# Kernel optimization log

Measured on AMD Instinct MI355X. Metric: run time of the kernel, lower is better.

## Reference

```python
import jax, jax.numpy as jnp
import numpy as np
from jax import lax

B, T = 64, 2048
ENC, DEC, ATT = 512, 1024, 128
NFILT, KSIZE = 32, 31
PAD = KSIZE // 2


def setup_inputs() -> dict:
    key = jax.random.key(0)
    ks = jax.random.split(key, 9)
    query = jax.random.normal(ks[0], (B, 1, DEC), dtype=jnp.float32)
    keys = jax.random.normal(ks[1], (B, T, ENC), dtype=jnp.float32)
    prev_weights = jax.random.uniform(ks[2], (B, T), dtype=jnp.float32)
    mask = jax.random.randint(ks[3], (B, T), 0, 2, dtype=jnp.int32)
    # params stored as [in, out] (transpose of torch Linear weight); same math
    W1 = jax.random.normal(ks[4], (ENC, ATT), dtype=jnp.float32) * (ENC ** -0.5)
    W2 = jax.random.normal(ks[5], (DEC, ATT), dtype=jnp.float32) * (DEC ** -0.5)
    V = jax.random.normal(ks[6], (ATT,), dtype=jnp.float32) * (ATT ** -0.5)
    conv_w = jax.random.normal(ks[7], (NFILT, 1, KSIZE), dtype=jnp.float32) * (KSIZE ** -0.5)
    loc_dense = jax.random.normal(ks[8], (NFILT, ATT), dtype=jnp.float32) * (NFILT ** -0.5)
    return {"query": query, "keys": keys, "prev_weights": prev_weights, "mask": mask,
            "W1": W1, "W2": W2, "V": V, "conv_w": conv_w, "loc_dense": loc_dense}


def reference(query, keys, prev_weights, mask, W1, W2, V, conv_w, loc_dense):
    proj_key = jnp.einsum('bte,ea->bta', keys, W1)          # [B,T,A]
    proj_query = jnp.einsum('bqd,da->bqa', query, W2)       # [B,1,A]
    # location conv: input [B,1,T], kernel [F,1,K], 'same' padding -> [B,F,T]
    loc_feat = lax.conv_general_dilated(prev_weights[:, None, :], conv_w,
                                        window_strides=(1,), padding=[(PAD, PAD)],
                                        dimension_numbers=('NCH', 'OIH', 'NCH'))
    proj_loc = jnp.einsum('bft,fa->bta', loc_feat, loc_dense)  # [B,T,A]
    scores = jnp.einsum('bta,a->bt', jnp.tanh(proj_key + proj_query + proj_loc), V)
    scores = jnp.where(mask == 0, -1e9, scores)
    weights = jax.nn.softmax(scores, axis=-1)                # [B,T]
    context = jnp.einsum('bt,bte->be', weights, keys)[:, None, :]  # [B,1,ENC]
    return context, weights
```

## Files before the change

### kernel.cpp

```cpp
#include <hip/hip_runtime.h>

typedef __attribute__((ext_vector_type(4))) float f32x4;
typedef __attribute__((ext_vector_type(8))) short bf16x8;

#define T_LEN 2048
#define ENC   512
#define DEC   1024
#define ATT   128
#define NB    64
#define BM    128
#define BK    32
#define NXB   (T_LEN / BM)
#define NSTEP 17

typedef unsigned int u32;
typedef __attribute__((address_space(1))) const u32 gu32;
typedef __attribute__((address_space(3))) u32 lu32;

__device__ __forceinline__ void async_copy16(const float* g, float* l) {
  __builtin_amdgcn_global_load_lds((gu32*)g, (lu32*)l, 16, 0, 0);
}

__device__ __forceinline__ unsigned short f2bf_rne(float x) {
  unsigned int u = __builtin_bit_cast(unsigned int, x);
  u += 0x7fff + ((u >> 16) & 1);
  return (unsigned short)(u >> 16);
}
__device__ __forceinline__ short f2bf_fast(float x) {
  unsigned int u = __builtin_bit_cast(unsigned int, x);
  return (short)((u + 0x8000u) >> 16);
}

__device__ __forceinline__ float fast_tanh(float x) {
  float e = __expf(2.f * x);
  return 1.f - 2.f / (e + 1.f);
}

__global__ __launch_bounds__(128) void prep(
    const float* __restrict__ query, const float* __restrict__ W2,
    const float* __restrict__ W1, const float* __restrict__ convw,
    const float* __restrict__ ldense,
    float* __restrict__ pq, unsigned short* __restrict__ Bl) {
  int bidx = blockIdx.x;
  if (bidx < NB) {
    int a = threadIdx.x;
    float acc = 0.f;
    for (int d = 0; d < DEC; ++d) acc += query[bidx * DEC + d] * W2[d * ATT + a];
    pq[bidx * ATT + a] = acc;
  } else {
    int a = bidx - NB;
    for (int k = threadIdx.x; k < NSTEP * BK; k += 128) {
      float v = 0.f;
      if (k < 512) {
        v = W1[k * ATT + a];
      } else if (k < 543) {
        int kc = k - 512;
        #pragma unroll
        for (int f = 0; f < 32; ++f) v += convw[f * 31 + kc] * ldense[f * ATT + a];
      }
      int kt = k >> 5, kk = k & 31;
      Bl[(kt * 128 + a) * BK + kk] = f2bf_rne(v);
    }
  }
}

__global__ __launch_bounds__(256, 4) void lsa_main(
    const float* __restrict__ keys, const float* __restrict__ prev,
    const int* __restrict__ mask, const unsigned short* __restrict__ Bl,
    const float* __restrict__ pq, const float* __restrict__ Vv,
    float* __restrict__ wout, float* __restrict__ dpart, float* __restrict__ cpart) {
  __shared__ float Abf[2][BM * BK];
  __shared__ float s_red[2][BM];
  __shared__ float e_vals[BM];

  const int tid = threadIdx.x;
  const int b = blockIdx.y;
  const int trow0 = blockIdx.x * BM;
  const int bid = b * NXB + blockIdx.x;

  const int lane = tid & 63;
  const int w = tid >> 6;
  const int wr = w >> 1, wc = w & 1;
  const int rsel = lane & 15, grp = lane >> 4;

  const int lr = lane >> 3, cp = lane & 7;
  const int gr = w * 32 + lr;
  const int gc = cp ^ lr;
  const float* gA = keys + ((size_t)b * T_LEN + trow0 + gr) * ENC + gc * 4;

  const unsigned short* gB = Bl + (size_t)(wc * 64 + rsel) * BK + grp * 8;

  const int rx = rsel & 7;
  const int ca0 = (2 * grp) ^ rx, ca1 = (2 * grp + 1) ^ rx;
  const int arow_base = (wr * 64 + rsel) * BK;

  f32x4 acc[4][4];
  #pragma unroll
  for (int m = 0; m < 4; ++m)
    #pragma unroll
    for (int n = 0; n < 4; ++n) acc[m][n] = (f32x4)0.f;

  #pragma unroll
  for (int i = 0; i < 4; ++i)
    async_copy16(gA + (size_t)i * 8 * ENC, &Abf[0][(w * 4 + i) * 256]);
  __syncthreads();

  for (int t = 0; t < 16; ++t) {
    if (t < 15) {
      const float* gt = gA + (t + 1) * BK;
      float* dst = &Abf[(t + 1) & 1][0];
      #pragma unroll
      for (int i = 0; i < 4; ++i)
        async_copy16(gt + (size_t)i * 8 * ENC, &dst[(w * 4 + i) * 256]);
    } else {
      const int r = tid >> 1, kh = tid & 1;
      const int rx2 = r & 7;
      float* dst = &Abf[0][r * BK];
      #pragma unroll
      for (int jc = 0; jc < 4; ++jc) {
        int c = kh * 4 + jc;
        f32x4 v;
        #pragma unroll
        for (int q = 0; q < 4; ++q) {
          int kk = c * 4 + q;
          int pos = trow0 + r + kk - 15;
          v[q] = (kk < 31 && pos >= 0 && pos < T_LEN) ? prev[b * T_LEN + pos] : 0.f;
        }
        *reinterpret_cast<f32x4*>(&dst[(c ^ rx2) * 4]) = v;
      }
    }
    bf16x8 bfr[4];
    {
      const unsigned short* gBt = gB + (size_t)t * (128 * BK);
      #pragma unroll
      for (int n = 0; n < 4; ++n)
        bfr[n] = *reinterpret_cast<const bf16x8*>(gBt + n * 16 * BK);
    }
    {
      const float* Ab = &Abf[t & 1][0];
      #pragma unroll
      for (int m = 0; m < 4; ++m) {
        f32x4 x0 = *reinterpret_cast<const f32x4*>(&Ab[arow_base + m * 16 * BK + ca0 * 4]);
        f32x4 x1 = *reinterpret_cast<const f32x4*>(&Ab[arow_base + m * 16 * BK + ca1 * 4]);
        bf16x8 af;
        #pragma unroll
        for (int j = 0; j < 4; ++j) { af[j] = f2bf_fast(x0[j]); af[4 + j] = f2bf_fast(x1[j]); }
        #pragma unroll
        for (int n = 0; n < 4; ++n)
          acc[m][n] = __builtin_amdgcn_mfma_f32_16x16x32_bf16(af, bfr[n], acc[m][n], 0, 0, 0);
      }
    }
    __syncthreads();
  }
  {
    bf16x8 bfr[4];
    const unsigned short* gBt = gB + (size_t)16 * (128 * BK);
    #pragma unroll
    for (int n = 0; n < 4; ++n)
      bfr[n] = *reinterpret_cast<const bf16x8*>(gBt + n * 16 * BK);
    const float* Ab = &Abf[0][0];
    #pragma unroll
    for (int m = 0; m < 4; ++m) {
      f32x4 x0 = *reinterpret_cast<const f32x4*>(&Ab[arow_base + m * 16 * BK + ca0 * 4]);
      f32x4 x1 = *reinterpret_cast<const f32x4*>(&Ab[arow_base + m * 16 * BK + ca1 * 4]);
      bf16x8 af;
      #pragma unroll
      for (int j = 0; j < 4; ++j) { af[j] = f2bf_fast(x0[j]); af[4 + j] = f2bf_fast(x1[j]); }
      #pragma unroll
      for (int n = 0; n < 4; ++n)
        acc[m][n] = __builtin_amdgcn_mfma_f32_16x16x32_bf16(af, bfr[n], acc[m][n], 0, 0, 0);
    }
  }

  float psum[4][4];
  #pragma unroll
  for (int m = 0; m < 4; ++m)
    #pragma unroll
    for (int i = 0; i < 4; ++i) psum[m][i] = 0.f;
  #pragma unroll
  for (int n = 0; n < 4; ++n) {
    int c = wc * 64 + n * 16 + rsel;
    float pqv = pq[b * ATT + c];
    float vv = Vv[c];
    #pragma unroll
    for (int m = 0; m < 4; ++m)
      #pragma unroll
      for (int i = 0; i < 4; ++i)
        psum[m][i] += vv * fast_tanh(acc[m][n][i] + pqv);
  }
  #pragma unroll
  for (int m = 0; m < 4; ++m)
    #pragma unroll
    for (int i = 0; i < 4; ++i) {
      float v = psum[m][i];
      v += __shfl_xor(v, 1, 64);
      v += __shfl_xor(v, 2, 64);
      v += __shfl_xor(v, 4, 64);
      v += __shfl_xor(v, 8, 64);
      psum[m][i] = v;
    }
  if (rsel == 0) {
    #pragma unroll
    for (int m = 0; m < 4; ++m)
      #pragma unroll
      for (int i = 0; i < 4; ++i)
        s_red[wc][wr * 64 + m * 16 + grp * 4 + i] = psum[m][i];
  }
  __syncthreads();

  if (tid < BM) {
    int trow = trow0 + tid;
    float s = s_red[0][tid] + s_red[1][tid];
    float e = (mask[b * T_LEN + trow] == 0) ? 0.f : __expf(s);
    wout[b * T_LEN + trow] = e;
    e_vals[tid] = e;
  }
  __syncthreads();

  if (tid < 64) {
    float v = e_vals[tid] + e_vals[tid + 64];
    #pragma unroll
    for (int off = 32; off; off >>= 1) v += __shfl_xor(v, off, 64);
    if (tid == 0) dpart[bid] = v;
  }

  float c0 = 0.f, c1 = 0.f;
  const float* krow = keys + ((size_t)b * T_LEN + trow0) * ENC;
  #pragma unroll 4
  for (int r = 0; r < BM; ++r) {
    float e = e_vals[r];
    if (e != 0.f) {
      c0 += e * krow[(size_t)r * ENC + tid];
      c1 += e * krow[(size_t)r * ENC + tid + 256];
    }
  }
  cpart[(size_t)bid * ENC + tid] = c0;
  cpart[(size_t)bid * ENC + tid + 256] = c1;
}

__global__ __launch_bounds__(256) void lsa_finalize(
    const float* __restrict__ dpart, const float* __restrict__ cpart,
    float* __restrict__ out) {
  int b = blockIdx.x, tid = threadIdx.x;
  float d = 0.f;
  #pragma unroll
  for (int i = 0; i < NXB; ++i) d += dpart[b * NXB + i];
  float inv = 1.f / d;
  for (int e = tid; e < ENC; e += 256) {
    float c = 0.f;
    #pragma unroll
    for (int i = 0; i < NXB; ++i) c += cpart[((size_t)(b * NXB + i)) * ENC + e];
    out[b * ENC + e] = c * inv;
  }
  float* wrow = out + NB * ENC + (size_t)b * T_LEN;
  for (int t = tid; t < T_LEN; t += 256) wrow[t] *= inv;
}

extern "C" void kernel_launch(void* const* d_in, const int* in_sizes, int n_in,
                              void* d_out, int out_size, void* d_ws, size_t ws_size,
                              hipStream_t stream) {
  const float* query  = (const float*)d_in[0];
  const float* keys   = (const float*)d_in[1];
  const float* prev   = (const float*)d_in[2];
  const int*   mask   = (const int*)d_in[3];
  const float* W1     = (const float*)d_in[4];
  const float* W2     = (const float*)d_in[5];
  const float* V      = (const float*)d_in[6];
  const float* convw  = (const float*)d_in[7];
  const float* ldense = (const float*)d_in[8];
  float* out = (float*)d_out;

  char* ws = (char*)d_ws;
  unsigned short* Bl = (unsigned short*)ws;
  float* pq    = (float*)(ws + 139264);
  float* dpart = (float*)(ws + 139264 + 32768);
  float* cpart = (float*)(ws + 139264 + 32768 + 4096);

  prep<<<dim3(192), dim3(128), 0, stream>>>(query, W2, W1, convw, ldense, pq, Bl);
  dim3 grid(NXB, NB);
  lsa_main<<<grid, dim3(256), 0, stream>>>(keys, prev, mask, Bl, pq, V,
                                           out + NB * ENC, dpart, cpart);
  lsa_finalize<<<dim3(NB), dim3(256), 0, stream>>>(dpart, cpart, out);
}
```

Before: 135.5 us.

## Triple-buffer A and B tiles in LDS with async loads and vmcnt waits

Moves the B (weight) tiles into LDS via async global-to-LDS copies, reorganises the packed bf16 weight layout to match, and switches the K loop to a three-stage pipeline that waits with explicit vmcnt counts instead of full barrier syncs. The context accumulation is rewritten to load float2 per thread without a branch on zero weights, and the query projection uses four independent accumulators. The aim is to hide global-load latency and cut redundant per-wave global B reads. In exchange, LDS use roughly doubles and the occupancy hint drops from 4 to 2 blocks per CU.

```diff
diff --git a/kernel.cpp b/kernel.cpp
--- a/kernel.cpp
+++ b/kernel.cpp
@@ -1,6 +1,7 @@
 #include <hip/hip_runtime.h>
 
 typedef __attribute__((ext_vector_type(4))) float f32x4;
+typedef __attribute__((ext_vector_type(2))) float f32x2;
 typedef __attribute__((ext_vector_type(8))) short bf16x8;
 
 #define T_LEN 2048
@@ -11,13 +12,12 @@
 #define BM    128
 #define BK    32
 #define NXB   (T_LEN / BM)
-#define NSTEP 17
 
 typedef unsigned int u32;
 typedef __attribute__((address_space(1))) const u32 gu32;
 typedef __attribute__((address_space(3))) u32 lu32;
 
-__device__ __forceinline__ void async_copy16(const float* g, float* l) {
+__device__ __forceinline__ void async_copy16(const void* g, void* l) {
   __builtin_amdgcn_global_load_lds((gu32*)g, (lu32*)l, 16, 0, 0);
 }
 
@@ -44,12 +44,18 @@
   int bidx = blockIdx.x;
   if (bidx < NB) {
     int a = threadIdx.x;
-    float acc = 0.f;
-    for (int d = 0; d < DEC; ++d) acc += query[bidx * DEC + d] * W2[d * ATT + a];
-    pq[bidx * ATT + a] = acc;
+    const float* q = query + bidx * DEC;
+    float a0 = 0.f, a1 = 0.f, a2 = 0.f, a3 = 0.f;
+    for (int d = 0; d < DEC; d += 4) {
+      a0 += q[d]     * W2[(d)     * ATT + a];
+      a1 += q[d + 1] * W2[(d + 1) * ATT + a];
+      a2 += q[d + 2] * W2[(d + 2) * ATT + a];
+      a3 += q[d + 3] * W2[(d + 3) * ATT + a];
+    }
+    pq[bidx * ATT + a] = (a0 + a1) + (a2 + a3);
   } else {
     int a = bidx - NB;
-    for (int k = threadIdx.x; k < NSTEP * BK; k += 128) {
+    for (int k = threadIdx.x; k < 17 * BK; k += 128) {
       float v = 0.f;
       if (k < 512) {
         v = W1[k * ATT + a];
@@ -59,17 +65,18 @@
         for (int f = 0; f < 32; ++f) v += convw[f * 31 + kc] * ldense[f * ATT + a];
       }
       int kt = k >> 5, kk = k & 31;
-      Bl[(kt * 128 + a) * BK + kk] = f2bf_rne(v);
-    }
-  }
-}
-
-__global__ __launch_bounds__(256, 4) void lsa_main(
+      Bl[(((kt * 4) + (kk >> 3)) * 128 + a) * 8 + (kk & 7)] = f2bf_rne(v);
+    }
+  }
+}
+
+__global__ __launch_bounds__(256, 2) void lsa_main(
     const float* __restrict__ keys, const float* __restrict__ prev,
     const int* __restrict__ mask, const unsigned short* __restrict__ Bl,
     const float* __restrict__ pq, const float* __restrict__ Vv,
     float* __restrict__ wout, float* __restrict__ dpart, float* __restrict__ cpart) {
-  __shared__ float Abf[2][BM * BK];
+  __shared__ float Abuf[3][BM * BK];
+  __shared__ unsigned short Bbuf[3][ATT * BK];
   __shared__ float s_red[2][BM];
   __shared__ float e_vals[BM];
 
@@ -84,81 +91,41 @@
   const int rsel = lane & 15, grp = lane >> 4;
 
   const int lr = lane >> 3, cp = lane & 7;
-  const int gr = w * 32 + lr;
   const int gc = cp ^ lr;
-  const float* gA = keys + ((size_t)b * T_LEN + trow0 + gr) * ENC + gc * 4;
-
-  const unsigned short* gB = Bl + (size_t)(wc * 64 + rsel) * BK + grp * 8;
+  const float* gA = keys + ((size_t)b * T_LEN + trow0 + w * 32 + lr) * ENC + gc * 4;
 
   const int rx = rsel & 7;
   const int ca0 = (2 * grp) ^ rx, ca1 = (2 * grp + 1) ^ rx;
   const int arow_base = (wr * 64 + rsel) * BK;
 
+  const int bcol_base = wc * 64 + rsel;
+
   f32x4 acc[4][4];
   #pragma unroll
   for (int m = 0; m < 4; ++m)
     #pragma unroll
     for (int n = 0; n < 4; ++n) acc[m][n] = (f32x4)0.f;
 
-  #pragma unroll
-  for (int i = 0; i < 4; ++i)
-    async_copy16(gA + (size_t)i * 8 * ENC, &Abf[0][(w * 4 + i) * 256]);
-  __syncthreads();
-
-  for (int t = 0; t < 16; ++t) {
-    if (t < 15) {
-      const float* gt = gA + (t + 1) * BK;
-      float* dst = &Abf[(t + 1) & 1][0];
-      #pragma unroll
-      for (int i = 0; i < 4; ++i)
-        async_copy16(gt + (size_t)i * 8 * ENC, &dst[(w * 4 + i) * 256]);
-    } else {
-      const int r = tid >> 1, kh = tid & 1;
-      const int rx2 = r & 7;
-      float* dst = &Abf[0][r * BK];
-      #pragma unroll
-      for (int jc = 0; jc < 4; ++jc) {
-        int c = kh * 4 + jc;
-        f32x4 v;
-        #pragma unroll
-        for (int q = 0; q < 4; ++q) {
-          int kk = c * 4 + q;
-          int pos = trow0 + r + kk - 15;
-          v[q] = (kk < 31 && pos >= 0 && pos < T_LEN) ? prev[b * T_LEN + pos] : 0.f;
-        }
-        *reinterpret_cast<f32x4*>(&dst[(c ^ rx2) * 4]) = v;
-      }
-    }
+  auto STAGE = [&](int t, int buf) {
+    const float* gt = gA + t * BK;
+    float* dstA = &Abuf[buf][0];
+    #pragma unroll
+    for (int i = 0; i < 4; ++i)
+      async_copy16(gt + (size_t)i * 8 * ENC, &dstA[(w * 4 + i) * 256]);
+    const unsigned short* gBt = Bl + (size_t)t * (ATT * BK) + w * 1024 + lane * 8;
+    unsigned short* dstB = &Bbuf[buf][0];
+    #pragma unroll
+    for (int j = 0; j < 2; ++j)
+      async_copy16(gBt + j * 512, &dstB[w * 1024 + j * 512]);
+  };
+
+  auto COMPUTE = [&](int buf) {
+    const unsigned short* Bb = &Bbuf[buf][0];
     bf16x8 bfr[4];
-    {
-      const unsigned short* gBt = gB + (size_t)t * (128 * BK);
-      #pragma unroll
-      for (int n = 0; n < 4; ++n)
-        bfr[n] = *reinterpret_cast<const bf16x8*>(gBt + n * 16 * BK);
-    }
-    {
-      const float* Ab = &Abf[t & 1][0];
-      #pragma unroll
-      for (int m = 0; m < 4; ++m) {
-        f32x4 x0 = *reinterpret_cast<const f32x4*>(&Ab[arow_base + m * 16 * BK + ca0 * 4]);
-        f32x4 x1 = *reinterpret_cast<const f32x4*>(&Ab[arow_base + m * 16 * BK + ca1 * 4]);
-        bf16x8 af;
-        #pragma unroll
-        for (int j = 0; j < 4; ++j) { af[j] = f2bf_fast(x0[j]); af[4 + j] = f2bf_fast(x1[j]); }
-        #pragma unroll
-        for (int n = 0; n < 4; ++n)
-          acc[m][n] = __builtin_amdgcn_mfma_f32_16x16x32_bf16(af, bfr[n], acc[m][n], 0, 0, 0);
-      }
-    }
-    __syncthreads();
-  }
-  {
-    bf16x8 bfr[4];
-    const unsigned short* gBt = gB + (size_t)16 * (128 * BK);
     #pragma unroll
     for (int n = 0; n < 4; ++n)
-      bfr[n] = *reinterpret_cast<const bf16x8*>(gBt + n * 16 * BK);
-    const float* Ab = &Abf[0][0];
+      bfr[n] = *reinterpret_cast<const bf16x8*>(&Bb[(grp * 128 + bcol_base + n * 16) * 8]);
+    const float* Ab = &Abuf[buf][0];
     #pragma unroll
     for (int m = 0; m < 4; ++m) {
       f32x4 x0 = *reinterpret_cast<const f32x4*>(&Ab[arow_base + m * 16 * BK + ca0 * 4]);
@@ -170,7 +137,50 @@
       for (int n = 0; n < 4; ++n)
         acc[m][n] = __builtin_amdgcn_mfma_f32_16x16x32_bf16(af, bfr[n], acc[m][n], 0, 0, 0);
     }
-  }
+  };
+
+  STAGE(0, 0);
+  STAGE(1, 1);
+  asm volatile("s_waitcnt vmcnt(6)" ::: "memory");
+  __builtin_amdgcn_s_barrier();
+  __builtin_amdgcn_sched_barrier(0);
+
+  #pragma unroll
+  for (int t = 0; t < 14; ++t) {
+    STAGE(t + 2, (t + 2) % 3);
+    COMPUTE(t % 3);
+    asm volatile("s_waitcnt vmcnt(6)" ::: "memory");
+    __builtin_amdgcn_s_barrier();
+    __builtin_amdgcn_sched_barrier(0);
+  }
+
+  {
+    const unsigned short* gBt = Bl + (size_t)16 * (ATT * BK) + w * 1024 + lane * 8;
+    unsigned short* dstB = &Bbuf[1][0];
+    #pragma unroll
+    for (int j = 0; j < 2; ++j)
+      async_copy16(gBt + j * 512, &dstB[w * 1024 + j * 512]);
+    const int r_ = tid >> 1, kh_ = tid & 1;
+    const int rx2_ = r_ & 7;
+    float* dstA = &Abuf[1][r_ * BK];
+    #pragma unroll
+    for (int jc = 0; jc < 4; ++jc) {
+      int c = kh_ * 4 + jc;
+      f32x4 v;
+      #pragma unroll
+      for (int q = 0; q < 4; ++q) {
+        int kk = c * 4 + q;
+        int pos = trow0 + r_ + kk - 15;
+        v[q] = (kk < 31 && pos >= 0 && pos < T_LEN) ? prev[b * T_LEN + pos] : 0.f;
+      }
+      *reinterpret_cast<f32x4*>(&dstA[(c ^ rx2_) * 4]) = v;
+    }
+    COMPUTE(14 % 3);
+    __syncthreads();
+  }
+
+  COMPUTE(15 % 3);
+  COMPUTE(16 % 3);
 
   float psum[4][4];
   #pragma unroll
@@ -224,18 +234,18 @@
     if (tid == 0) dpart[bid] = v;
   }
 
-  float c0 = 0.f, c1 = 0.f;
-  const float* krow = keys + ((size_t)b * T_LEN + trow0) * ENC;
-  #pragma unroll 4
-  for (int r = 0; r < BM; ++r) {
-    float e = e_vals[r];
-    if (e != 0.f) {
-      c0 += e * krow[(size_t)r * ENC + tid];
-      c1 += e * krow[(size_t)r * ENC + tid + 256];
-    }
-  }
-  cpart[(size_t)bid * ENC + tid] = c0;
-  cpart[(size_t)bid * ENC + tid + 256] = c1;
+  {
+    const float* kcol = keys + ((size_t)b * T_LEN + trow0) * ENC + 2 * tid;
+    f32x2 cacc; cacc.x = 0.f; cacc.y = 0.f;
+    #pragma unroll 8
+    for (int r = 0; r < BM; ++r) {
+      float e = e_vals[r];
+      f32x2 kv = *reinterpret_cast<const f32x2*>(kcol + (size_t)r * ENC);
+      cacc.x += e * kv.x;
+      cacc.y += e * kv.y;
+    }
+    *reinterpret_cast<f32x2*>(cpart + (size_t)bid * ENC + 2 * tid) = cacc;
+  }
 }
 
 __global__ __launch_bounds__(256) void lsa_finalize(
```

After: 130.0 us, median of 2. 4.0% less time.
